# Optimization experiments

Hardware: AMD Instinct MI355X
Metric: run time of the kernel (lower is better)

## Reference

```python
import jax, jax.numpy as jnp
import numpy as np

N = 50000
D = 128           # feature_dim
H = 8             # num_heads
DH = D // H       # head_dim = 16
K = 32            # k_neighbors
FFN = int(D * 1.5)  # 192
TAU_NEG = 0.6
BETA = 1.5
LN_EPS = 1e-5


def layer_norm(x, g, b):
    mu = jnp.mean(x, axis=-1, keepdims=True)
    var = jnp.mean((x - mu) ** 2, axis=-1, keepdims=True)
    return (x - mu) * jax.lax.rsqrt(var + LN_EPS) * g + b


def setup_inputs() -> dict:
    key = jax.random.key(0)
    ks = jax.random.split(key, 12)
    s = 1.0 / np.sqrt(D)
    inp = {
        "features": jax.random.normal(ks[0], (N, D), dtype=jnp.float32),
        "knn_indices": jax.random.randint(ks[1], (N, K), 0, N, dtype=jnp.int64 if jax.config.jax_enable_x64 else jnp.int32),
        "spatial_distances": jax.random.uniform(ks[2], (N, K), dtype=jnp.float32) * 8.0,
        "Wq": jax.random.normal(ks[3], (D, D), dtype=jnp.float32) * s,
        "Wk": jax.random.normal(ks[4], (D, D), dtype=jnp.float32) * s,
        "Wv": jax.random.normal(ks[5], (D, D), dtype=jnp.float32) * s,
        "Wo": jax.random.normal(ks[6], (D, D), dtype=jnp.float32) * s,
        "bo": jnp.zeros((D,), dtype=jnp.float32),
        "ln1_g": jnp.ones((D,), dtype=jnp.float32),
        "ln1_b": jnp.zeros((D,), dtype=jnp.float32),
        "W1": jax.random.normal(ks[7], (D, FFN), dtype=jnp.float32) * s,
        "b1": jnp.zeros((FFN,), dtype=jnp.float32),
        "W2": jax.random.normal(ks[8], (FFN, D), dtype=jnp.float32) * (1.0 / np.sqrt(FFN)),
        "b2": jnp.zeros((D,), dtype=jnp.float32),
        "ln2_g": jnp.ones((D,), dtype=jnp.float32),
        "ln2_b": jnp.zeros((D,), dtype=jnp.float32),
    }
    return inp


def reference(features, knn_indices, spatial_distances, Wq, Wk, Wv, Wo, bo,
              ln1_g, ln1_b, W1, b1, W2, b2, ln2_g, ln2_b):
    n = features.shape[0]
    Q = (features @ Wq).reshape(n, H, DH)           # (N,H,dh)
    Kp = (features @ Wk).reshape(n, H, DH)
    Vp = (features @ Wv).reshape(n, H, DH)

    K_local = Kp[knn_indices]                        # (N,K,H,dh) irregular gather
    V_local = Vp[knn_indices]                        # (N,K,H,dh)

    raw_scores = jnp.einsum("nhd,nkhd->nhk", Q, K_local) / np.sqrt(DH)  # (N,H,K)

    # per-head spatial decay: 1 / 2^(h+1)
    head_scalings = (0.5 ** jnp.arange(1, H + 1, dtype=features.dtype))  # (H,)
    scaled_dist = spatial_distances[:, None, :] * head_scalings[None, :, None]  # (N,H,K)

    attn_pos = jax.nn.softmax(raw_scores - scaled_dist, axis=-1)
    attn_neg = jax.nn.softmax((-raw_scores - scaled_dist) / TAU_NEG, axis=-1)
    attn = attn_pos - BETA * attn_neg                # (N,H,K); dropout is identity in eval

    attended = jnp.einsum("nhk,nkhd->nhd", attn, V_local).reshape(n, D)

    x = attended @ Wo + bo + features
    x = layer_norm(x, ln1_g, ln1_b)

    h = jax.nn.gelu(x @ W1 + b1, approximate=False)
    ffn_out = h @ W2 + b2
    out = layer_norm(ffn_out + x, ln2_g, ln2_b)
    return out
```

## Files before the change

kernel.cpp:

```cpp
#include <hip/hip_runtime.h>
#include <cmath>

typedef __attribute__((ext_vector_type(8))) short bf16x8;
typedef __attribute__((ext_vector_type(4))) float f32x4;

__device__ __forceinline__ unsigned short f2bf(float x) {
    unsigned int u = __float_as_uint(x);
    u += 0x7fffu + ((u >> 16) & 1u);
    return (unsigned short)(u >> 16);
}
__device__ __forceinline__ unsigned int pk2(float a, float b) {
    return (unsigned int)f2bf(a) | ((unsigned int)f2bf(b) << 16);
}
__device__ __forceinline__ float bflo(unsigned int u) { return __uint_as_float(u << 16); }
__device__ __forceinline__ float bfhi(unsigned int u) { return __uint_as_float(u & 0xffff0000u); }
__device__ __forceinline__ float gelu_exact(float v) {
    return 0.5f * v * (1.0f + erff(v * 0.70710678118654752440f));
}
__device__ __forceinline__ void unp16(const uint4& a, const uint4& b, float* q) {
    q[0]=bflo(a.x);  q[1]=bfhi(a.x);  q[2]=bflo(a.y);  q[3]=bfhi(a.y);
    q[4]=bflo(a.z);  q[5]=bfhi(a.z);  q[6]=bflo(a.w);  q[7]=bfhi(a.w);
    q[8]=bflo(b.x);  q[9]=bfhi(b.x);  q[10]=bflo(b.y); q[11]=bfhi(b.y);
    q[12]=bflo(b.z); q[13]=bfhi(b.z); q[14]=bflo(b.w); q[15]=bfhi(b.w);
}

__global__ __launch_bounds__(256, 1) void k_prep(
    const float* __restrict__ Wq, const float* __restrict__ Wk, const float* __restrict__ Wv,
    const float* __restrict__ Wo, const float* __restrict__ W1, const float* __restrict__ W2,
    unsigned short* __restrict__ wsz)
{
    int f = blockIdx.x * 256 + threadIdx.x;
    const float* W; unsigned short* dst; int M, KS, fl;
    if (f < 2048)       { W = Wq; dst = wsz;         M = 128; KS = 4; fl = f; }
    else if (f < 4096)  { W = Wk; dst = wsz + 16384; M = 128; KS = 4; fl = f - 2048; }
    else if (f < 6144)  { W = Wv; dst = wsz + 32768; M = 128; KS = 4; fl = f - 4096; }
    else if (f < 8192)  { W = Wo; dst = wsz + 49152; M = 128; KS = 4; fl = f - 6144; }
    else if (f < 11264) { W = W1; dst = wsz + 65536; M = 192; KS = 4; fl = f - 8192; }
    else if (f < 14336) { W = W2; dst = wsz + 90112; M = 128; KS = 6; fl = f - 11264; }
    else return;
    const int l  = fl & 63;
    const int ks = (fl >> 6) % KS;
    const int ct = (fl >> 6) / KS;
    const int k0 = ks * 32 + (l >> 4) * 8;
    const int col = ct * 16 + (l & 15);
    unsigned short tmp[8];
    #pragma unroll
    for (int j = 0; j < 8; ++j) tmp[j] = f2bf(W[(size_t)(k0 + j) * M + col]);
    ((uint4*)dst)[fl] = *(uint4*)tmp;
}

__global__ __launch_bounds__(512, 1) void k_qkv(
    const float* __restrict__ feat, const unsigned short* __restrict__ wsz,
    unsigned short* __restrict__ Qb, unsigned short* __restrict__ Kb,
    unsigned short* __restrict__ Vb, int n)
{
    __shared__ __align__(16) unsigned short wld[16384];
    __shared__ __align__(16) unsigned short at[128 * 136];
    const int tid = threadIdx.x;
    const int row0 = blockIdx.x * 128;

    for (int i = tid; i < 4096; i += 512) {
        int row = i >> 5, col = (i & 31) * 4;
        float4 v = make_float4(0.f, 0.f, 0.f, 0.f);
        int gr = row0 + row;
        if (gr < n) v = ((const float4*)(feat + (size_t)gr * 128))[i & 31];
        *((uint2*)&at[row * 136 + col]) = make_uint2(pk2(v.x, v.y), pk2(v.z, v.w));
    }

    const int w = tid >> 6, lane = tid & 63;
    const int lrow = lane & 15, kgrp = lane >> 4;
    const int node = row0 + w * 16 + lrow;
    bf16x8 bfr[4];

    for (int mat = 0; mat < 3; ++mat) {
        for (int i = tid; i < 2048; i += 512)
            ((uint4*)wld)[i] = ((const uint4*)(wsz + mat * 16384))[i];
        __syncthreads();
        if (mat == 0) {
            #pragma unroll
            for (int ks = 0; ks < 4; ++ks)
                bfr[ks] = *(const bf16x8*)&at[(w * 16 + lrow) * 136 + ks * 32 + kgrp * 8];
        }
        f32x4 acc[8];
        #pragma unroll
        for (int ct = 0; ct < 8; ++ct) acc[ct] = (f32x4){0.f, 0.f, 0.f, 0.f};
        #pragma unroll
        for (int ct = 0; ct < 8; ++ct)
            #pragma unroll
            for (int ks = 0; ks < 4; ++ks) {
                bf16x8 afr = *(const bf16x8*)&wld[((ct * 4 + ks) * 64 + lane) * 8];
                acc[ct] = __builtin_amdgcn_mfma_f32_16x16x32_bf16(afr, bfr[ks], acc[ct], 0, 0, 0);
            }
        unsigned short* O = (mat == 0) ? Qb : (mat == 1 ? Kb : Vb);
        if (node < n) {
            #pragma unroll
            for (int ct = 0; ct < 8; ++ct) {
                int col = ct * 16 + kgrp * 4;
                *((uint2*)(O + (size_t)node * 128 + col)) =
                    make_uint2(pk2(acc[ct][0], acc[ct][1]), pk2(acc[ct][2], acc[ct][3]));
            }
        }
        __syncthreads();
    }
}

__global__ __launch_bounds__(256, 1) void k_attn(
    const unsigned short* __restrict__ Qb, const unsigned short* __restrict__ Kb,
    const unsigned short* __restrict__ Vb,
    const int* __restrict__ knn, const float* __restrict__ dist,
    unsigned short* __restrict__ attb, int n)
{
    const int lane = threadIdx.x & 63;
    const int node = blockIdx.x * 4 + (threadIdx.x >> 6);
    if (node >= n) return;
    const int h = lane >> 3, r = lane & 7;

    const unsigned short* qp = Qb + (size_t)node * 128 + h * 16;
    uint4 qa = *(const uint4*)qp;
    uint4 qb = *(const uint4*)(qp + 8);
    float q[16];
    unp16(qa, qb, q);
    const float hs = exp2f(-(float)(h + 1));

    int idx[4]; float sd[4];
    #pragma unroll
    for (int jj = 0; jj < 4; ++jj) {
        int j = r + jj * 8;
        idx[jj] = knn[(size_t)node * 32 + j];
        sd[jj]  = dist[(size_t)node * 32 + j] * hs;
    }

    uint4 k0[4], k1[4], v0[4], v1[4];
    #pragma unroll
    for (int jj = 0; jj < 4; ++jj) {
        const unsigned short* kp = Kb + (size_t)idx[jj] * 128 + h * 16;
        k0[jj] = *(const uint4*)kp;
        k1[jj] = *(const uint4*)(kp + 8);
    }
    #pragma unroll
    for (int jj = 0; jj < 4; ++jj) {
        const unsigned short* vp = Vb + (size_t)idx[jj] * 128 + h * 16;
        v0[jj] = *(const uint4*)vp;
        v1[jj] = *(const uint4*)(vp + 8);
    }

    float ap[4], an[4];
    #pragma unroll
    for (int jj = 0; jj < 4; ++jj) {
        float kv[16];
        unp16(k0[jj], k1[jj], kv);
        float s = 0.f;
        #pragma unroll
        for (int i = 0; i < 16; ++i) s = fmaf(q[i], kv[i], s);
        float raw = s * 0.25f;
        ap[jj] = raw - sd[jj];
        an[jj] = (-raw - sd[jj]) * (1.0f / 0.6f);
    }

    float mp = fmaxf(fmaxf(ap[0], ap[1]), fmaxf(ap[2], ap[3]));
    float mn = fmaxf(fmaxf(an[0], an[1]), fmaxf(an[2], an[3]));
    #pragma unroll
    for (int msk = 1; msk < 8; msk <<= 1) {
        mp = fmaxf(mp, __shfl_xor(mp, msk, 8));
        mn = fmaxf(mn, __shfl_xor(mn, msk, 8));
    }
    float ep[4], en[4], sp = 0.f, sn = 0.f;
    #pragma unroll
    for (int jj = 0; jj < 4; ++jj) {
        ep[jj] = expf(ap[jj] - mp); sp += ep[jj];
        en[jj] = expf(an[jj] - mn); sn += en[jj];
    }
    #pragma unroll
    for (int msk = 1; msk < 8; msk <<= 1) {
        sp += __shfl_xor(sp, msk, 8);
        sn += __shfl_xor(sn, msk, 8);
    }
    const float isp = 1.0f / sp;
    const float isn = 1.5f / sn;

    float acc[16];
    #pragma unroll
    for (int i = 0; i < 16; ++i) acc[i] = 0.f;
    #pragma unroll
    for (int jj = 0; jj < 4; ++jj) {
        float wgt = ep[jj] * isp - en[jj] * isn;
        float vv[16];
        unp16(v0[jj], v1[jj], vv);
        #pragma unroll
        for (int i = 0; i < 16; ++i) acc[i] = fmaf(wgt, vv[i], acc[i]);
    }
    #pragma unroll
    for (int i = 0; i < 16; ++i) {
        #pragma unroll
        for (int msk = 1; msk < 8; msk <<= 1) acc[i] += __shfl_xor(acc[i], msk, 8);
    }
    if (r == 0) {
        unsigned int o[8];
        #pragma unroll
        for (int i = 0; i < 8; ++i) o[i] = pk2(acc[2 * i], acc[2 * i + 1]);
        unsigned short* op = attb + (size_t)node * 128 + h * 16;
        *((uint4*)op)     = make_uint4(o[0], o[1], o[2], o[3]);
        *((uint4*)(op+8)) = make_uint4(o[4], o[5], o[6], o[7]);
    }
}

__global__ __launch_bounds__(256, 1) void k_tail(
    const unsigned short* __restrict__ attb, const float* __restrict__ feat,
    const unsigned short* __restrict__ wsz,
    const float* __restrict__ bo, const float* __restrict__ g1, const float* __restrict__ b1ln,
    const float* __restrict__ b1f, const float* __restrict__ b2f,
    const float* __restrict__ g2, const float* __restrict__ b2ln,
    float* __restrict__ out, int n, int tiles)
{
    __shared__ __align__(16) unsigned short wo_s[16384];
    __shared__ __align__(16) unsigned short w1_s[24576];
    __shared__ __align__(16) unsigned short w2_s[24576];
    __shared__ __align__(16) unsigned short act[64 * 200];
    const int tid = threadIdx.x;

    for (int i = tid; i < 2048; i += 256) ((uint4*)wo_s)[i] = ((const uint4*)(wsz + 49152))[i];
    for (int i = tid; i < 3072; i += 256) ((uint4*)w1_s)[i] = ((const uint4*)(wsz + 65536))[i];
    for (int i = tid; i < 3072; i += 256) ((uint4*)w2_s)[i] = ((const uint4*)(wsz + 90112))[i];

    const int w = tid >> 6, lane = tid & 63;
    const int lrow = lane & 15, kgrp = lane >> 4;
    const int lbase = (w * 16 + lrow) * 200;

    for (int t = blockIdx.x; t < tiles; t += gridDim.x) {
        const int row0 = t * 64;
        const int node = row0 + w * 16 + lrow;
        const bool valid = node < n;
        __syncthreads();
        for (int i = tid; i < 1024; i += 256) {
            int row = i >> 4, cg = i & 15;
            int gr = row0 + row;
            uint4 v = make_uint4(0u, 0u, 0u, 0u);
            if (gr < n) v = *(const uint4*)(attb + (size_t)gr * 128 + cg * 8);
            *((uint4*)&act[row * 200 + cg * 8]) = v;
        }
        __syncthreads();

        bf16x8 bfr[6];
        #pragma unroll
        for (int ks = 0; ks < 4; ++ks)
            bfr[ks] = *(const bf16x8*)&act[lbase + ks * 32 + kgrp * 8];
        f32x4 X[8];
        #pragma unroll
        for (int ct = 0; ct < 8; ++ct) {
            X[ct] = (f32x4){0.f, 0.f, 0.f, 0.f};
            #pragma unroll
            for (int ks = 0; ks < 4; ++ks) {
                bf16x8 afr = *(const bf16x8*)&wo_s[((ct * 4 + ks) * 64 + lane) * 8];
                X[ct] = __builtin_amdgcn_mfma_f32_16x16x32_bf16(afr, bfr[ks], X[ct], 0, 0, 0);
            }
        }
        #pragma unroll
        for (int ct = 0; ct < 8; ++ct) {
            int col = ct * 16 + kgrp * 4;
            float4 bv = *((const float4*)(bo + col));
            float4 fr = make_float4(0.f, 0.f, 0.f, 0.f);
            if (valid) fr = *((const float4*)(feat + (size_t)node * 128 + col));
            X[ct][0] += bv.x + fr.x; X[ct][1] += bv.y + fr.y;
            X[ct][2] += bv.z + fr.z; X[ct][3] += bv.w + fr.w;
        }
        float s = 0.f;
        #pragma unroll
        for (int ct = 0; ct < 8; ++ct) s += X[ct][0] + X[ct][1] + X[ct][2] + X[ct][3];
        s += __shfl_xor(s, 16); s += __shfl_xor(s, 32);
        const float mu1 = s * (1.0f / 128.0f);
        float s2 = 0.f;
        #pragma unroll
        for (int ct = 0; ct < 8; ++ct)
            #pragma unroll
            for (int rr = 0; rr < 4; ++rr) { float d = X[ct][rr] - mu1; s2 = fmaf(d, d, s2); }
        s2 += __shfl_xor(s2, 16); s2 += __shfl_xor(s2, 32);
        const float rs1 = rsqrtf(s2 * (1.0f / 128.0f) + 1e-5f);
        f32x4 XN[8];
        #pragma unroll
        for (int ct = 0; ct < 8; ++ct) {
            int col = ct * 16 + kgrp * 4;
            float4 gg = *((const float4*)(g1 + col));
            float4 bb = *((const float4*)(b1ln + col));
            XN[ct][0] = (X[ct][0] - mu1) * rs1 * gg.x + bb.x;
            XN[ct][1] = (X[ct][1] - mu1) * rs1 * gg.y + bb.y;
            XN[ct][2] = (X[ct][2] - mu1) * rs1 * gg.z + bb.z;
            XN[ct][3] = (X[ct][3] - mu1) * rs1 * gg.w + bb.w;
        }
        __syncthreads();
        #pragma unroll
        for (int ct = 0; ct < 8; ++ct) {
            int col = ct * 16 + kgrp * 4;
            *((uint2*)&act[lbase + col]) =
                make_uint2(pk2(XN[ct][0], XN[ct][1]), pk2(XN[ct][2], XN[ct][3]));
        }
        __syncthreads();

        #pragma unroll
        for (int ks = 0; ks < 4; ++ks)
            bfr[ks] = *(const bf16x8*)&act[lbase + ks * 32 + kgrp * 8];
        f32x4 Hc[12];
        #pragma unroll
        for (int ct = 0; ct < 12; ++ct) {
            Hc[ct] = (f32x4){0.f, 0.f, 0.f, 0.f};
            #pragma unroll
            for (int ks = 0; ks < 4; ++ks) {
                bf16x8 afr = *(const bf16x8*)&w1_s[((ct * 4 + ks) * 64 + lane) * 8];
                Hc[ct] = __builtin_amdgcn_mfma_f32_16x16x32_bf16(afr, bfr[ks], Hc[ct], 0, 0, 0);
            }
        }
        #pragma unroll
        for (int ct = 0; ct < 12; ++ct) {
            int col = ct * 16 + kgrp * 4;
            float4 bv = *((const float4*)(b1f + col));
            Hc[ct][0] = gelu_exact(Hc[ct][0] + bv.x);
            Hc[ct][1] = gelu_exact(Hc[ct][1] + bv.y);
            Hc[ct][2] = gelu_exact(Hc[ct][2] + bv.z);
            Hc[ct][3] = gelu_exact(Hc[ct][3] + bv.w);
        }
        __syncthreads();
        #pragma unroll
        for (int ct = 0; ct < 12; ++ct) {
            int col = ct * 16 + kgrp * 4;
            *((uint2*)&act[lbase + col]) =
                make_uint2(pk2(Hc[ct][0], Hc[ct][1]), pk2(Hc[ct][2], Hc[ct][3]));
        }
        __syncthreads();

        #pragma unroll
        for (int ks = 0; ks < 6; ++ks)
            bfr[ks] = *(const bf16x8*)&act[lbase + ks * 32 + kgrp * 8];
        f32x4 Y[8];
        #pragma unroll
        for (int ct = 0; ct < 8; ++ct) {
            Y[ct] = (f32x4){0.f, 0.f, 0.f, 0.f};
            #pragma unroll
            for (int ks = 0; ks < 6; ++ks) {
                bf16x8 afr = *(const bf16x8*)&w2_s[((ct * 6 + ks) * 64 + lane) * 8];
                Y[ct] = __builtin_amdgcn_mfma_f32_16x16x32_bf16(afr, bfr[ks], Y[ct], 0, 0, 0);
            }
        }
        #pragma unroll
        for (int ct = 0; ct < 8; ++ct) {
            int col = ct * 16 + kgrp * 4;
            float4 bv = *((const float4*)(b2f + col));
            Y[ct][0] += bv.x + XN[ct][0]; Y[ct][1] += bv.y + XN[ct][1];
            Y[ct][2] += bv.z + XN[ct][2]; Y[ct][3] += bv.w + XN[ct][3];
        }
        float t1 = 0.f;
        #pragma unroll
        for (int ct = 0; ct < 8; ++ct) t1 += Y[ct][0] + Y[ct][1] + Y[ct][2] + Y[ct][3];
        t1 += __shfl_xor(t1, 16); t1 += __shfl_xor(t1, 32);
        const float mu2 = t1 * (1.0f / 128.0f);
        float t2 = 0.f;
        #pragma unroll
        for (int ct = 0; ct < 8; ++ct)
            #pragma unroll
            for (int rr = 0; rr < 4; ++rr) { float d = Y[ct][rr] - mu2; t2 = fmaf(d, d, t2); }
        t2 += __shfl_xor(t2, 16); t2 += __shfl_xor(t2, 32);
        const float rs2 = rsqrtf(t2 * (1.0f / 128.0f) + 1e-5f);
        if (valid) {
            #pragma unroll
            for (int ct = 0; ct < 8; ++ct) {
                int col = ct * 16 + kgrp * 4;
                float4 gg = *((const float4*)(g2 + col));
                float4 bb = *((const float4*)(b2ln + col));
                float4 o;
                o.x = (Y[ct][0] - mu2) * rs2 * gg.x + bb.x;
                o.y = (Y[ct][1] - mu2) * rs2 * gg.y + bb.y;
                o.z = (Y[ct][2] - mu2) * rs2 * gg.z + bb.z;
                o.w = (Y[ct][3] - mu2) * rs2 * gg.w + bb.w;
                *((float4*)(out + (size_t)node * 128 + col)) = o;
            }
        }
    }
}

extern "C" void kernel_launch(void* const* d_in, const int* in_sizes, int n_in,
                              void* d_out, int out_size, void* d_ws, size_t ws_size,
                              hipStream_t stream)
{
    const float* feat = (const float*)d_in[0];
    const int*   knn  = (const int*)d_in[1];
    const float* dist = (const float*)d_in[2];
    const float* Wq   = (const float*)d_in[3];
    const float* Wk   = (const float*)d_in[4];
    const float* Wv   = (const float*)d_in[5];
    const float* Wo   = (const float*)d_in[6];
    const float* bo   = (const float*)d_in[7];
    const float* g1   = (const float*)d_in[8];
    const float* b1ln = (const float*)d_in[9];
    const float* W1   = (const float*)d_in[10];
    const float* b1f  = (const float*)d_in[11];
    const float* W2   = (const float*)d_in[12];
    const float* b2f  = (const float*)d_in[13];
    const float* g2   = (const float*)d_in[14];
    const float* b2ln = (const float*)d_in[15];
    float* out = (float*)d_out;

    const int n = in_sizes[0] / 128;
    const size_t ND = (size_t)n * 128;
    if (ws_size < 8 * ND + 262144) return;

    unsigned short* Qb   = (unsigned short*)d_ws;
    unsigned short* Kb   = Qb + ND;
    unsigned short* Vb   = Kb + ND;
    unsigned short* attb = Vb + ND;
    unsigned short* Wsz  = attb + ND;

    const int tiles64 = (n + 63) / 64;
    k_prep<<<56, 256, 0, stream>>>(Wq, Wk, Wv, Wo, W1, W2, Wsz);
    k_qkv <<<(n + 127) / 128, 512, 0, stream>>>(feat, Wsz, Qb, Kb, Vb, n);
    k_attn<<<(n + 3) / 4, 256, 0, stream>>>(Qb, Kb, Vb, knn, dist, attb, n);
    k_tail<<<256, 256, 0, stream>>>(attb, feat, Wsz, bo, g1, b1ln, b1f, b2f, g2, b2ln,
                                    out, n, tiles64);
}
```

Measured before the change: 198.2 us.

## Switch to fp16 with packed half math and split tail into three kernels

Replaces bf16 storage and MFMA with fp16 throughout. The attention dot products and weighted V accumulation now use packed __half2 FMAs, including the cross-lane reduction. The QKV kernel now reads weights straight from global memory instead of staging them in LDS, and it uses smaller blocks with a higher occupancy bound. The persistent fused tail kernel is split into three grid-wide kernels (Wo+LN1, FFN1, FFN2+LN2) that pass fp16 intermediates through reused workspace buffers. This adds extra global round trips and launches, and it risks fp16 precision and overflow issues in the attention accumulation.

```diff
diff --git a/kernel.cpp b/kernel.cpp
--- a/kernel.cpp
+++ b/kernel.cpp
@@ -1,27 +1,21 @@
 #include <hip/hip_runtime.h>
+#include <hip/hip_fp16.h>
 #include <cmath>
 
-typedef __attribute__((ext_vector_type(8))) short bf16x8;
+typedef __attribute__((ext_vector_type(8))) _Float16 f16x8;
 typedef __attribute__((ext_vector_type(4))) float f32x4;
 
-__device__ __forceinline__ unsigned short f2bf(float x) {
-    unsigned int u = __float_as_uint(x);
-    u += 0x7fffu + ((u >> 16) & 1u);
-    return (unsigned short)(u >> 16);
-}
-__device__ __forceinline__ unsigned int pk2(float a, float b) {
-    return (unsigned int)f2bf(a) | ((unsigned int)f2bf(b) << 16);
-}
-__device__ __forceinline__ float bflo(unsigned int u) { return __uint_as_float(u << 16); }
-__device__ __forceinline__ float bfhi(unsigned int u) { return __uint_as_float(u & 0xffff0000u); }
+__device__ __forceinline__ unsigned int pkh(float a, float b) {
+    __half2 h = __floats2half2_rn(a, b);
+    return *(unsigned int*)&h;
+}
 __device__ __forceinline__ float gelu_exact(float v) {
     return 0.5f * v * (1.0f + erff(v * 0.70710678118654752440f));
 }
-__device__ __forceinline__ void unp16(const uint4& a, const uint4& b, float* q) {
-    q[0]=bflo(a.x);  q[1]=bfhi(a.x);  q[2]=bflo(a.y);  q[3]=bfhi(a.y);
-    q[4]=bflo(a.z);  q[5]=bfhi(a.z);  q[6]=bflo(a.w);  q[7]=bfhi(a.w);
-    q[8]=bflo(b.x);  q[9]=bfhi(b.x);  q[10]=bflo(b.y); q[11]=bfhi(b.y);
-    q[12]=bflo(b.z); q[13]=bfhi(b.z); q[14]=bflo(b.w); q[15]=bfhi(b.w);
+__device__ __forceinline__ __half2 shfl8h(__half2 x, int m) {
+    int xi = *(int*)&x;
+    int yi = __shfl_xor(xi, m, 8);
+    return *(__half2*)&yi;
 }
 
 __global__ __launch_bounds__(256, 1) void k_prep(
@@ -45,42 +39,40 @@
     const int col = ct * 16 + (l & 15);
     unsigned short tmp[8];
     #pragma unroll
-    for (int j = 0; j < 8; ++j) tmp[j] = f2bf(W[(size_t)(k0 + j) * M + col]);
+    for (int j = 0; j < 8; ++j) {
+        __half hh = __float2half(W[(size_t)(k0 + j) * M + col]);
+        tmp[j] = *(unsigned short*)&hh;
+    }
     ((uint4*)dst)[fl] = *(uint4*)tmp;
 }
 
-__global__ __launch_bounds__(512, 1) void k_qkv(
+__global__ __launch_bounds__(256, 4) void k_qkv(
     const float* __restrict__ feat, const unsigned short* __restrict__ wsz,
     unsigned short* __restrict__ Qb, unsigned short* __restrict__ Kb,
     unsigned short* __restrict__ Vb, int n)
 {
-    __shared__ __align__(16) unsigned short wld[16384];
-    __shared__ __align__(16) unsigned short at[128 * 136];
-    const int tid = threadIdx.x;
-    const int row0 = blockIdx.x * 128;
-
-    for (int i = tid; i < 4096; i += 512) {
-        int row = i >> 5, col = (i & 31) * 4;
-        float4 v = make_float4(0.f, 0.f, 0.f, 0.f);
-        int gr = row0 + row;
-        if (gr < n) v = ((const float4*)(feat + (size_t)gr * 128))[i & 31];
-        *((uint2*)&at[row * 136 + col]) = make_uint2(pk2(v.x, v.y), pk2(v.z, v.w));
-    }
-
-    const int w = tid >> 6, lane = tid & 63;
+    const int w = threadIdx.x >> 6, lane = threadIdx.x & 63;
     const int lrow = lane & 15, kgrp = lane >> 4;
-    const int node = row0 + w * 16 + lrow;
-    bf16x8 bfr[4];
+    const int node = blockIdx.x * 64 + w * 16 + lrow;
+    const bool valid = node < n;
+
+    f16x8 bfr[4];
+    #pragma unroll
+    for (int ks = 0; ks < 4; ++ks) {
+        float4 lo = make_float4(0.f, 0.f, 0.f, 0.f), hi = lo;
+        if (valid) {
+            const float* p = feat + (size_t)node * 128 + ks * 32 + kgrp * 8;
+            lo = *(const float4*)p;
+            hi = *(const float4*)(p + 4);
+        }
+        f16x8 b;
+        b[0] = (_Float16)lo.x; b[1] = (_Float16)lo.y; b[2] = (_Float16)lo.z; b[3] = (_Float16)lo.w;
+        b[4] = (_Float16)hi.x; b[5] = (_Float16)hi.y; b[6] = (_Float16)hi.z; b[7] = (_Float16)hi.w;
+        bfr[ks] = b;
+    }
 
     for (int mat = 0; mat < 3; ++mat) {
-        for (int i = tid; i < 2048; i += 512)
-            ((uint4*)wld)[i] = ((const uint4*)(wsz + mat * 16384))[i];
-        __syncthreads();
-        if (mat == 0) {
-            #pragma unroll
-            for (int ks = 0; ks < 4; ++ks)
-                bfr[ks] = *(const bf16x8*)&at[(w * 16 + lrow) * 136 + ks * 32 + kgrp * 8];
-        }
+        const unsigned short* wb = wsz + mat * 16384;
         f32x4 acc[8];
         #pragma unroll
         for (int ct = 0; ct < 8; ++ct) acc[ct] = (f32x4){0.f, 0.f, 0.f, 0.f};
@@ -88,23 +80,22 @@
         for (int ct = 0; ct < 8; ++ct)
             #pragma unroll
             for (int ks = 0; ks < 4; ++ks) {
-                bf16x8 afr = *(const bf16x8*)&wld[((ct * 4 + ks) * 64 + lane) * 8];
-                acc[ct] = __builtin_amdgcn_mfma_f32_16x16x32_bf16(afr, bfr[ks], acc[ct], 0, 0, 0);
+                f16x8 afr = *(const f16x8*)(wb + ((size_t)(ct * 4 + ks) * 64 + lane) * 8);
+                acc[ct] = __builtin_amdgcn_mfma_f32_16x16x32_f16(afr, bfr[ks], acc[ct], 0, 0, 0);
             }
         unsigned short* O = (mat == 0) ? Qb : (mat == 1 ? Kb : Vb);
-        if (node < n) {
+        if (valid) {
             #pragma unroll
             for (int ct = 0; ct < 8; ++ct) {
                 int col = ct * 16 + kgrp * 4;
                 *((uint2*)(O + (size_t)node * 128 + col)) =
-                    make_uint2(pk2(acc[ct][0], acc[ct][1]), pk2(acc[ct][2], acc[ct][3]));
+                    make_uint2(pkh(acc[ct][0], acc[ct][1]), pkh(acc[ct][2], acc[ct][3]));
             }
         }
-        __syncthreads();
-    }
-}
-
-__global__ __launch_bounds__(256, 1) void k_attn(
+    }
+}
+
+__global__ __launch_bounds__(256, 4) void k_attn(
     const unsigned short* __restrict__ Qb, const unsigned short* __restrict__ Kb,
     const unsigned short* __restrict__ Vb,
     const int* __restrict__ knn, const float* __restrict__ dist,
@@ -114,12 +105,6 @@
     const int node = blockIdx.x * 4 + (threadIdx.x >> 6);
     if (node >= n) return;
     const int h = lane >> 3, r = lane & 7;
-
-    const unsigned short* qp = Qb + (size_t)node * 128 + h * 16;
-    uint4 qa = *(const uint4*)qp;
-    uint4 qb = *(const uint4*)(qp + 8);
-    float q[16];
-    unp16(qa, qb, q);
     const float hs = exp2f(-(float)(h + 1));
 
     int idx[4]; float sd[4];
@@ -130,6 +115,11 @@
         sd[jj]  = dist[(size_t)node * 32 + j] * hs;
     }
 
+    const unsigned short* qp = Qb + (size_t)node * 128 + h * 16;
+    __half2 q2[8];
+    *((uint4*)&q2[0]) = *(const uint4*)qp;
+    *((uint4*)&q2[4]) = *(const uint4*)(qp + 8);
+
     uint4 k0[4], k1[4], v0[4], v1[4];
     #pragma unroll
     for (int jj = 0; jj < 4; ++jj) {
@@ -147,11 +137,17 @@
     float ap[4], an[4];
     #pragma unroll
     for (int jj = 0; jj < 4; ++jj) {
-        float kv[16];
-        unp16(k0[jj], k1[jj], kv);
-        float s = 0.f;
-        #pragma unroll
-        for (int i = 0; i < 16; ++i) s = fmaf(q[i], kv[i], s);
+        const __half2* ka = (const __half2*)&k0[jj];
+        const __half2* kb = (const __half2*)&k1[jj];
+        __half2 s0 = __hmul2(q2[0], ka[0]);
+        s0 = __hfma2(q2[1], ka[1], s0);
+        s0 = __hfma2(q2[2], ka[2], s0);
+        s0 = __hfma2(q2[3], ka[3], s0);
+        __half2 s1 = __hmul2(q2[4], kb[0]);
+        s1 = __hfma2(q2[5], kb[1], s1);
+        s1 = __hfma2(q2[6], kb[2], s1);
+        s1 = __hfma2(q2[7], kb[3], s1);
+        float s = __low2float(s0) + __high2float(s0) + __low2float(s1) + __high2float(s1);
         float raw = s * 0.25f;
         ap[jj] = raw - sd[jj];
         an[jj] = (-raw - sd[jj]) * (1.0f / 0.6f);
@@ -178,199 +174,226 @@
     const float isp = 1.0f / sp;
     const float isn = 1.5f / sn;
 
-    float acc[16];
-    #pragma unroll
-    for (int i = 0; i < 16; ++i) acc[i] = 0.f;
+    __half2 acc2[8];
+    #pragma unroll
+    for (int i = 0; i < 8; ++i) acc2[i] = __float2half2_rn(0.f);
     #pragma unroll
     for (int jj = 0; jj < 4; ++jj) {
         float wgt = ep[jj] * isp - en[jj] * isn;
-        float vv[16];
-        unp16(v0[jj], v1[jj], vv);
-        #pragma unroll
-        for (int i = 0; i < 16; ++i) acc[i] = fmaf(wgt, vv[i], acc[i]);
-    }
-    #pragma unroll
-    for (int i = 0; i < 16; ++i) {
-        #pragma unroll
-        for (int msk = 1; msk < 8; msk <<= 1) acc[i] += __shfl_xor(acc[i], msk, 8);
+        __half2 w2 = __float2half2_rn(wgt);
+        const __half2* va = (const __half2*)&v0[jj];
+        const __half2* vb = (const __half2*)&v1[jj];
+        acc2[0] = __hfma2(w2, va[0], acc2[0]);
+        acc2[1] = __hfma2(w2, va[1], acc2[1]);
+        acc2[2] = __hfma2(w2, va[2], acc2[2]);
+        acc2[3] = __hfma2(w2, va[3], acc2[3]);
+        acc2[4] = __hfma2(w2, vb[0], acc2[4]);
+        acc2[5] = __hfma2(w2, vb[1], acc2[5]);
+        acc2[6] = __hfma2(w2, vb[2], acc2[6]);
+        acc2[7] = __hfma2(w2, vb[3], acc2[7]);
+    }
+    #pragma unroll
+    for (int i = 0; i < 8; ++i) {
+        acc2[i] = __hadd2(acc2[i], shfl8h(acc2[i], 1));
+        acc2[i] = __hadd2(acc2[i], shfl8h(acc2[i], 2));
+        acc2[i] = __hadd2(acc2[i], shfl8h(acc2[i], 4));
     }
     if (r == 0) {
-        unsigned int o[8];
-        #pragma unroll
-        for (int i = 0; i < 8; ++i) o[i] = pk2(acc[2 * i], acc[2 * i + 1]);
         unsigned short* op = attb + (size_t)node * 128 + h * 16;
-        *((uint4*)op)     = make_uint4(o[0], o[1], o[2], o[3]);
-        *((uint4*)(op+8)) = make_uint4(o[4], o[5], o[6], o[7]);
-    }
-}
-
-__global__ __launch_bounds__(256, 1) void k_tail(
+        *((uint4*)op)       = *(uint4*)&acc2[0];
+        *((uint4*)(op + 8)) = *(uint4*)&acc2[4];
+    }
+}
+
+__global__ __launch_bounds__(512, 1) void k_tail1(
     const unsigned short* __restrict__ attb, const float* __restrict__ feat,
     const unsigned short* __restrict__ wsz,
     const float* __restrict__ bo, const float* __restrict__ g1, const float* __restrict__ b1ln,
-    const float* __restrict__ b1f, const float* __restrict__ b2f,
-    const float* __restrict__ g2, const float* __restrict__ b2ln,
-    float* __restrict__ out, int n, int tiles)
+    unsigned short* __restrict__ Xb, int n)
 {
     __shared__ __align__(16) unsigned short wo_s[16384];
-    __shared__ __align__(16) unsigned short w1_s[24576];
-    __shared__ __align__(16) unsigned short w2_s[24576];
-    __shared__ __align__(16) unsigned short act[64 * 200];
     const int tid = threadIdx.x;
-
-    for (int i = tid; i < 2048; i += 256) ((uint4*)wo_s)[i] = ((const uint4*)(wsz + 49152))[i];
-    for (int i = tid; i < 3072; i += 256) ((uint4*)w1_s)[i] = ((const uint4*)(wsz + 65536))[i];
-    for (int i = tid; i < 3072; i += 256) ((uint4*)w2_s)[i] = ((const uint4*)(wsz + 90112))[i];
+    for (int i = tid; i < 2048; i += 512)
+        ((uint4*)wo_s)[i] = ((const uint4*)(wsz + 49152))[i];
 
     const int w = tid >> 6, lane = tid & 63;
     const int lrow = lane & 15, kgrp = lane >> 4;
-    const int lbase = (w * 16 + lrow) * 200;
-
-    for (int t = blockIdx.x; t < tiles; t += gridDim.x) {
-        const int row0 = t * 64;
-        const int node = row0 + w * 16 + lrow;
-        const bool valid = node < n;
-        __syncthreads();
-        for (int i = tid; i < 1024; i += 256) {
-            int row = i >> 4, cg = i & 15;
-            int gr = row0 + row;
-            uint4 v = make_uint4(0u, 0u, 0u, 0u);
-            if (gr < n) v = *(const uint4*)(attb + (size_t)gr * 128 + cg * 8);
-            *((uint4*)&act[row * 200 + cg * 8]) = v;
-        }
-        __syncthreads();
-
-        bf16x8 bfr[6];
-        #pragma unroll
-        for (int ks = 0; ks < 4; ++ks)
-            bfr[ks] = *(const bf16x8*)&act[lbase + ks * 32 + kgrp * 8];
-        f32x4 X[8];
-        #pragma unroll
-        for (int ct = 0; ct < 8; ++ct) {
-            X[ct] = (f32x4){0.f, 0.f, 0.f, 0.f};
-            #pragma unroll
-            for (int ks = 0; ks < 4; ++ks) {
-                bf16x8 afr = *(const bf16x8*)&wo_s[((ct * 4 + ks) * 64 + lane) * 8];
-                X[ct] = __builtin_amdgcn_mfma_f32_16x16x32_bf16(afr, bfr[ks], X[ct], 0, 0, 0);
-            }
-        }
-        #pragma unroll
-        for (int ct = 0; ct < 8; ++ct) {
-            int col = ct * 16 + kgrp * 4;
-            float4 bv = *((const float4*)(bo + col));
-            float4 fr = make_float4(0.f, 0.f, 0.f, 0.f);
-            if (valid) fr = *((const float4*)(feat + (size_t)node * 128 + col));
-            X[ct][0] += bv.x + fr.x; X[ct][1] += bv.y + fr.y;
-            X[ct][2] += bv.z + fr.z; X[ct][3] += bv.w + fr.w;
-        }
-        float s = 0.f;
-        #pragma unroll
-        for (int ct = 0; ct < 8; ++ct) s += X[ct][0] + X[ct][1] + X[ct][2] + X[ct][3];
-        s += __shfl_xor(s, 16); s += __shfl_xor(s, 32);
-        const float mu1 = s * (1.0f / 128.0f);
-        float s2 = 0.f;
-        #pragma unroll
-        for (int ct = 0; ct < 8; ++ct)
-            #pragma unroll
-            for (int rr = 0; rr < 4; ++rr) { float d = X[ct][rr] - mu1; s2 = fmaf(d, d, s2); }
-        s2 += __shfl_xor(s2, 16); s2 += __shfl_xor(s2, 32);
-        const float rs1 = rsqrtf(s2 * (1.0f / 128.0f) + 1e-5f);
-        f32x4 XN[8];
+    const int node = blockIdx.x * 128 + w * 16 + lrow;
+    const bool valid = node < n;
+
+    f16x8 bfr[4];
+    #pragma unroll
+    for (int ks = 0; ks < 4; ++ks) {
+        uint4 u = make_uint4(0u, 0u, 0u, 0u);
+        if (valid) u = *(const uint4*)(attb + (size_t)node * 128 + ks * 32 + kgrp * 8);
+        bfr[ks] = *(f16x8*)&u;
+    }
+    __syncthreads();
+
+    f32x4 X[8];
+    #pragma unroll
+    for (int ct = 0; ct < 8; ++ct) {
+        X[ct] = (f32x4){0.f, 0.f, 0.f, 0.f};
+        #pragma unroll
+        for (int ks = 0; ks < 4; ++ks) {
+            f16x8 afr = *(const f16x8*)&wo_s[((ct * 4 + ks) * 64 + lane) * 8];
+            X[ct] = __builtin_amdgcn_mfma_f32_16x16x32_f16(afr, bfr[ks], X[ct], 0, 0, 0);
+        }
+    }
+    #pragma unroll
+    for (int ct = 0; ct < 8; ++ct) {
+        int col = ct * 16 + kgrp * 4;
+        float4 bv = *((const float4*)(bo + col));
+        float4 fr = make_float4(0.f, 0.f, 0.f, 0.f);
+        if (valid) fr = *((const float4*)(feat + (size_t)node * 128 + col));
+        X[ct][0] += bv.x + fr.x; X[ct][1] += bv.y + fr.y;
+        X[ct][2] += bv.z + fr.z; X[ct][3] += bv.w + fr.w;
+    }
+    float s = 0.f;
+    #pragma unroll
+    for (int ct = 0; ct < 8; ++ct) s += X[ct][0] + X[ct][1] + X[ct][2] + X[ct][3];
+    s += __shfl_xor(s, 16); s += __shfl_xor(s, 32);
+    const float mu = s * (1.0f / 128.0f);
+    float s2 = 0.f;
+    #pragma unroll
+    for (int ct = 0; ct < 8; ++ct)
+        #pragma unroll
+        for (int rr = 0; rr < 4; ++rr) { float d = X[ct][rr] - mu; s2 = fmaf(d, d, s2); }
+    s2 += __shfl_xor(s2, 16); s2 += __shfl_xor(s2, 32);
+    const float rs = rsqrtf(s2 * (1.0f / 128.0f) + 1e-5f);
+    if (valid) {
         #pragma unroll
         for (int ct = 0; ct < 8; ++ct) {
             int col = ct * 16 + kgrp * 4;
             float4 gg = *((const float4*)(g1 + col));
             float4 bb = *((const float4*)(b1ln + col));
-            XN[ct][0] = (X[ct][0] - mu1) * rs1 * gg.x + bb.x;
-            XN[ct][1] = (X[ct][1] - mu1) * rs1 * gg.y + bb.y;
-            XN[ct][2] = (X[ct][2] - mu1) * rs1 * gg.z + bb.z;
-            XN[ct][3] = (X[ct][3] - mu1) * rs1 * gg.w + bb.w;
-        }
-        __syncthreads();
-        #pragma unroll
-        for (int ct = 0; ct < 8; ++ct) {
-            int col = ct * 16 + kgrp * 4;
-            *((uint2*)&act[lbase + col]) =
-                make_uint2(pk2(XN[ct][0], XN[ct][1]), pk2(XN[ct][2], XN[ct][3]));
-        }
-        __syncthreads();
-
-        #pragma unroll
-        for (int ks = 0; ks < 4; ++ks)
-            bfr[ks] = *(const bf16x8*)&act[lbase + ks * 32 + kgrp * 8];
-        f32x4 Hc[12];
-        #pragma unroll
-        for (int ct = 0; ct < 12; ++ct) {
-            Hc[ct] = (f32x4){0.f, 0.f, 0.f, 0.f};
-            #pragma unroll
-            for (int ks = 0; ks < 4; ++ks) {
-                bf16x8 afr = *(const bf16x8*)&w1_s[((ct * 4 + ks) * 64 + lane) * 8];
-                Hc[ct] = __builtin_amdgcn_mfma_f32_16x16x32_bf16(afr, bfr[ks], Hc[ct], 0, 0, 0);
-            }
-        }
+            float x0 = (X[ct][0] - mu) * rs * gg.x + bb.x;
+            float x1 = (X[ct][1] - mu) * rs * gg.y + bb.y;
+            float x2 = (X[ct][2] - mu) * rs * gg.z + bb.z;
+            float x3 = (X[ct][3] - mu) * rs * gg.w + bb.w;
+            *((uint2*)(Xb + (size_t)node * 128 + col)) = make_uint2(pkh(x0, x1), pkh(x2, x3));
+        }
+    }
+}
+
+__global__ __launch_bounds__(512, 1) void k_ffn1(
+    const unsigned short* __restrict__ Xb, const unsigned short* __restrict__ wsz,
+    const float* __restrict__ b1f, unsigned short* __restrict__ Hb, int n)
+{
+    __shared__ __align__(16) unsigned short w1_s[24576];
+    const int tid = threadIdx.x;
+    for (int i = tid; i < 3072; i += 512)
+        ((uint4*)w1_s)[i] = ((const uint4*)(wsz + 65536))[i];
+
+    const int w = tid >> 6, lane = tid & 63;
+    const int lrow = lane & 15, kgrp = lane >> 4;
+    const int node = blockIdx.x * 128 + w * 16 + lrow;
+    const bool valid = node < n;
+
+    f16x8 bfr[4];
+    #pragma unroll
+    for (int ks = 0; ks < 4; ++ks) {
+        uint4 u = make_uint4(0u, 0u, 0u, 0u);
+        if (valid) u = *(const uint4*)(Xb + (size_t)node * 128 + ks * 32 + kgrp * 8);
+        bfr[ks] = *(f16x8*)&u;
+    }
+    __syncthreads();
+
+    f32x4 acc[12];
+    #pragma unroll
+    for (int ct = 0; ct < 12; ++ct) {
+        acc[ct] = (f32x4){0.f, 0.f, 0.f, 0.f};
+        #pragma unroll
+        for (int ks = 0; ks < 4; ++ks) {
+            f16x8 afr = *(const f16x8*)&w1_s[((ct * 4 + ks) * 64 + lane) * 8];
+            acc[ct] = __builtin_amdgcn_mfma_f32_16x16x32_f16(afr, bfr[ks], acc[ct], 0, 0, 0);
+        }
+    }
+    if (valid) {
         #pragma unroll
         for (int ct = 0; ct < 12; ++ct) {
             int col = ct * 16 + kgrp * 4;
             float4 bv = *((const float4*)(b1f + col));
-            Hc[ct][0] = gelu_exact(Hc[ct][0] + bv.x);
-            Hc[ct][1] = gelu_exact(Hc[ct][1] + bv.y);
-            Hc[ct][2] = gelu_exact(Hc[ct][2] + bv.z);
-            Hc[ct][3] = gelu_exact(Hc[ct][3] + bv.w);
-        }
-        __syncthreads();
-        #pragma unroll
-        for (int ct = 0; ct < 12; ++ct) {
-            int col = ct * 16 + kgrp * 4;
-            *((uint2*)&act[lbase + col]) =
-                make_uint2(pk2(Hc[ct][0], Hc[ct][1]), pk2(Hc[ct][2], Hc[ct][3]));
-        }
-        __syncthreads();
-
-        #pragma unroll
-        for (int ks = 0; ks < 6; ++ks)
-            bfr[ks] = *(const bf16x8*)&act[lbase + ks * 32 + kgrp * 8];
-        f32x4 Y[8];
-        #pragma unroll
-        for (int ct = 0; ct < 8; ++ct) {
-            Y[ct] = (f32x4){0.f, 0.f, 0.f, 0.f};
-            #pragma unroll
-            for (int ks = 0; ks < 6; ++ks) {
-                bf16x8 afr = *(const bf16x8*)&w2_s[((ct * 6 + ks) * 64 + lane) * 8];
-                Y[ct] = __builtin_amdgcn_mfma_f32_16x16x32_bf16(afr, bfr[ks], Y[ct], 0, 0, 0);
-            }
-        }
+            float h0 = gelu_exact(acc[ct][0] + bv.x);
+            float h1 = gelu_exact(acc[ct][1] + bv.y);
+            float h2 = gelu_exact(acc[ct][2] + bv.z);
+            float h3 = gelu_exact(acc[ct][3] + bv.w);
+            *((uint2*)(Hb + (size_t)node * 192 + col)) = make_uint2(pkh(h0, h1), pkh(h2, h3));
+        }
+    }
+}
+
+__global__ __launch_bounds__(512, 1) void k_ffn2(
+    const unsigned short* __restrict__ Hb, const unsigned short* __restrict__ Xb,
+    const unsigned short* __restrict__ wsz, const float* __restrict__ b2f,
+    const float* __restrict__ g2, const float* __restrict__ b2ln,
+    float* __restrict__ out, int n)
+{
+    __shared__ __align__(16) unsigned short w2_s[24576];
+    const int tid = threadIdx.x;
+    for (int i = tid; i < 3072; i += 512)
+        ((uint4*)w2_s)[i] = ((const uint4*)(wsz + 90112))[i];
+
+    const int w = tid >> 6, lane = tid & 63;
+    const int lrow = lane & 15, kgrp = lane >> 4;
+    const int node = blockIdx.x * 128 + w * 16 + lrow;
+    const bool valid = node < n;
+
+    f16x8 bfr[6];
+    #pragma unroll
+    for (int ks = 0; ks < 6; ++ks) {
+        uint4 u = make_uint4(0u, 0u, 0u, 0u);
+        if (valid) u = *(const uint4*)(Hb + (size_t)node * 192 + ks * 32 + kgrp * 8);
+        bfr[ks] = *(f16x8*)&u;
+    }
+    __syncthreads();
+
+    f32x4 Y[8];
+    #pragma unroll
+    for (int ct = 0; ct < 8; ++ct) {
+        Y[ct] = (f32x4){0.f, 0.f, 0.f, 0.f};
+        #pragma unroll
+        for (int ks = 0; ks < 6; ++ks) {
+            f16x8 afr = *(const f16x8*)&w2_s[((ct * 6 + ks) * 64 + lane) * 8];
+            Y[ct] = __builtin_amdgcn_mfma_f32_16x16x32_f16(afr, bfr[ks], Y[ct], 0, 0, 0);
+        }
+    }
+    #pragma unroll
+    for (int ct = 0; ct < 8; ++ct) {
+        int col = ct * 16 + kgrp * 4;
+        float4 bv = *((const float4*)(b2f + col));
+        uint2 xr = make_uint2(0u, 0u);
+        if (valid) xr = *((const uint2*)(Xb + (size_t)node * 128 + col));
+        __half2 x01 = *(__half2*)&xr.x, x23 = *(__half2*)&xr.y;
+        Y[ct][0] += bv.x + __low2float(x01);
+        Y[ct][1] += bv.y + __high2float(x01);
+        Y[ct][2] += bv.z + __low2float(x23);
+        Y[ct][3] += bv.w + __high2float(x23);
+    }
+    float s = 0.f;
+    #pragma unroll
+    for (int ct = 0; ct < 8; ++ct) s += Y[ct][0] + Y[ct][1] + Y[ct][2] + Y[ct][3];
+    s += __shfl_xor(s, 16); s += __shfl_xor(s, 32);
+    const float mu = s * (1.0f / 128.0f);
+    float s2 = 0.f;
+    #pragma unroll
+    for (int ct = 0; ct < 8; ++ct)
+        #pragma unroll
+        for (int rr = 0; rr < 4; ++rr) { float d = Y[ct][rr] - mu; s2 = fmaf(d, d, s2); }
+    s2 += __shfl_xor(s2, 16); s2 += __shfl_xor(s2, 32);
+    const float rs = rsqrtf(s2 * (1.0f / 128.0f) + 1e-5f);
+    if (valid) {
         #pragma unroll
         for (int ct = 0; ct < 8; ++ct) {
             int col = ct * 16 + kgrp * 4;
-            float4 bv = *((const float4*)(b2f + col));
-            Y[ct][0] += bv.x + XN[ct][0]; Y[ct][1] += bv.y + XN[ct][1];
-            Y[ct][2] += bv.z + XN[ct][2]; Y[ct][3] += bv.w + XN[ct][3];
-        }
-        float t1 = 0.f;
-        #pragma unroll
-        for (int ct = 0; ct < 8; ++ct) t1 += Y[ct][0] + Y[ct][1] + Y[ct][2] + Y[ct][3];
-        t1 += __shfl_xor(t1, 16); t1 += __shfl_xor(t1, 32);
-        const float mu2 = t1 * (1.0f / 128.0f);
-        float t2 = 0.f;
-        #pragma unroll
-        for (int ct = 0; ct < 8; ++ct)
-            #pragma unroll
-            for (int rr = 0; rr < 4; ++rr) { float d = Y[ct][rr] - mu2; t2 = fmaf(d, d, t2); }
-        t2 += __shfl_xor(t2, 16); t2 += __shfl_xor(t2, 32);
-        const float rs2 = rsqrtf(t2 * (1.0f / 128.0f) + 1e-5f);
-        if (valid) {
-            #pragma unroll
-            for (int ct = 0; ct < 8; ++ct) {
-                int col = ct * 16 + kgrp * 4;
-                float4 gg = *((const float4*)(g2 + col));
-                float4 bb = *((const float4*)(b2ln + col));
-                float4 o;
-                o.x = (Y[ct][0] - mu2) * rs2 * gg.x + bb.x;
-                o.y = (Y[ct][1] - mu2) * rs2 * gg.y + bb.y;
-                o.z = (Y[ct][2] - mu2) * rs2 * gg.z + bb.z;
-                o.w = (Y[ct][3] - mu2) * rs2 * gg.w + bb.w;
-                *((float4*)(out + (size_t)node * 128 + col)) = o;
-            }
+            float4 gg = *((const float4*)(g2 + col));
+            float4 bb = *((const float4*)(b2ln + col));
+            float4 o;
+            o.x = (Y[ct][0] - mu) * rs * gg.x + bb.x;
+            o.y = (Y[ct][1] - mu) * rs * gg.y + bb.y;
+            o.z = (Y[ct][2] - mu) * rs * gg.z + bb.z;
+            o.w = (Y[ct][3] - mu) * rs * gg.w + bb.w;
+            *((float4*)(out + (size_t)node * 128 + col)) = o;
         }
     }
 }
@@ -406,11 +429,13 @@
     unsigned short* Vb   = Kb + ND;
     unsigned short* attb = Vb + ND;
     unsigned short* Wsz  = attb + ND;
-
-    const int tiles64 = (n + 63) / 64;
-    k_prep<<<56, 256, 0, stream>>>(Wq, Wk, Wv, Wo, W1, W2, Wsz);
-    k_qkv <<<(n + 127) / 128, 512, 0, stream>>>(feat, Wsz, Qb, Kb, Vb, n);
-    k_attn<<<(n + 3) / 4, 256, 0, stream>>>(Qb, Kb, Vb, knn, dist, attb, n);
-    k_tail<<<256, 256, 0, stream>>>(attb, feat, Wsz, bo, g1, b1ln, b1f, b2f, g2, b2ln,
-                                    out, n, tiles64);
-}
+    unsigned short* Xb   = Vb;
+    unsigned short* Hb   = Qb;
+
+    k_prep <<<56, 256, 0, stream>>>(Wq, Wk, Wv, Wo, W1, W2, Wsz);
+    k_qkv  <<<(n + 63) / 64,   256, 0, stream>>>(feat, Wsz, Qb, Kb, Vb, n);
+    k_attn <<<(n + 3) / 4,     256, 0, stream>>>(Qb, Kb, Vb, knn, dist, attb, n);
+    k_tail1<<<(n + 127) / 128, 512, 0, stream>>>(attb, feat, Wsz, bo, g1, b1ln, Xb, n);
+    k_ffn1 <<<(n + 127) / 128, 512, 0, stream>>>(Xb, Wsz, b1f, Hb, n);
+    k_ffn2 <<<(n + 127) / 128, 512, 0, stream>>>(Hb, Xb, Wsz, b2f, g2, b2ln, out, n);
+}
```

Result: faster. 191.0 us (-3.6%).
